# Kernel optimization log

Hardware: AMD Instinct MI355X
Metric: run time of the kernel (lower is better)

Reference implementation:

```python
import jax, jax.numpy as jnp
import numpy as np

ND = 64       # dijetFeatures (channels)
NPAIR = 6     # six dijet slots


def _interleave(x, d):
    # x: [n, nd, 12] -> [n, nd, 6, 2]; d: [n, nd, 6] -> [n, nd, 6, 1]
    n, nd, _ = x.shape
    xr = x.reshape(n, nd, NPAIR, 2)
    z = jnp.concatenate([xr, d[..., None]], axis=-1)  # [n, nd, 6, 3]
    return z


def _conv_s3(z, W, b):
    # z: [n, in, 6, 3] grouped windows; W: [out, in, 3]; stride-3 k-3 conv == per-window contraction
    return jnp.einsum('bisk,oik->bos', z, W) + b[None, :, None]  # [n, out, 6]


def setup_inputs() -> dict:
    key = jax.random.key(0)
    ks = jax.random.split(key, 8)
    n = 65536
    inp = {
        'x': jax.random.normal(ks[0], (n, ND, 12), dtype=jnp.float32),
        'd': jax.random.normal(ks[1], (n, ND, NPAIR), dtype=jnp.float32),
        'W1': jax.random.normal(ks[2], (ND, ND, 3), dtype=jnp.float32) * 0.05,
        'b1': jax.random.normal(ks[3], (ND,), dtype=jnp.float32) * 0.05,
        'W2': jax.random.normal(ks[4], (ND, ND, 3), dtype=jnp.float32) * 0.05,
        'b2': jax.random.normal(ks[5], (ND,), dtype=jnp.float32) * 0.05,
        'W3': jax.random.normal(ks[6], (ND, ND, 3), dtype=jnp.float32) * 0.05,
        'b3': jax.random.normal(ks[7], (ND,), dtype=jnp.float32) * 0.05,
    }
    return inp


def reference(x, d, W1, b1, W2, b2, W3, b3):
    d1 = d
    d = jax.nn.relu(_conv_s3(_interleave(x, d), W1, b1))
    d = jax.nn.relu(_conv_s3(_interleave(x, d), W2, b2))
    d = _conv_s3(_interleave(x, d), W3, b3)
    return jax.nn.relu(d + d1)
```

## Files before the change

### kernel.cpp

```cpp
#include <hip/hip_runtime.h>

#define ND 64
#define NPAIR 6

typedef short bf16x8 __attribute__((ext_vector_type(8)));
typedef float floatx4 __attribute__((ext_vector_type(4)));

static constexpr int SPB  = 8;
static constexpr int ROWS = SPB * NPAIR;

__device__ __forceinline__ unsigned short f2bf(float f) {
    unsigned u = __builtin_bit_cast(unsigned, f);
    u += 0x7FFFu + ((u >> 16) & 1u);
    return (unsigned short)(u >> 16);
}
__device__ __forceinline__ unsigned f2bf2(float lo, float hi) {
    return (unsigned)f2bf(lo) | ((unsigned)f2bf(hi) << 16);
}
__device__ __forceinline__ unsigned relupack2(float a, float ba, float b, float bb) {
    float u = a + ba; u = u > 0.f ? u : 0.f;
    float v = b + bb; v = v > 0.f ? v : 0.f;
    return f2bf2(u, v);
}
__device__ __forceinline__ int swzAx(int row, int c) { return (c & 8) | ((c ^ row) & 7); }
__device__ __forceinline__ int swzD (int row, int c) { return (c ^ row) & 7; }

__global__ void repack_w(const float* __restrict__ W1, const float* __restrict__ W2,
                         const float* __restrict__ W3, unsigned short* __restrict__ P) {
    int idx = blockIdx.x * 256 + threadIdx.x;
    if (idx >= 3 * 4 * 6 * 64 * 8) return;
    int j    = idx & 7;
    int lane = (idx >> 3) & 63;
    int g    = idx >> 9;
    int c    = g % 6;
    int ot   = (g / 6) & 3;
    int L    = g / 24;
    int m = lane & 15, q = lane >> 4;
    int ch = 32 * (ot >> 1) + 8 * (m >> 2) + 4 * (ot & 1) + (m & 3);
    int k  = c * 32 + q * 8 + j;
    const float* W = (L == 0) ? W1 : (L == 1) ? W2 : W3;
    float v = (k < 128) ? W[ch * 192 + (k >> 1) * 3 + (k & 1)]
                        : W[ch * 192 + (k - 128) * 3 + 2];
    P[idx] = f2bf(v);
}

__global__ __launch_bounds__(192, 5) void dijet_main(
    const float* __restrict__ x, const float* __restrict__ d,
    const float* __restrict__ b1, const float* __restrict__ b2,
    const float* __restrict__ b3, const unsigned short* __restrict__ Wa,
    float* __restrict__ out)
{
    __shared__ __align__(16) unsigned short SMEM[ROWS * 128 + ROWS * 64];
    unsigned short* Xs = SMEM;
    unsigned short* Ds = SMEM + ROWS * 128;
    float* Co = (float*)SMEM;

    const int t   = threadIdx.x;
    const int b0  = blockIdx.x * SPB;
    const int wv  = t >> 6;
    const int lane = t & 63;
    const int l15 = lane & 15;
    const int q   = lane >> 4;

    float2 dres[8];
    {
        const float2* d2 = (const float2*)(d + (size_t)b0 * 384);
        #pragma unroll
        for (int m = 0; m < 8; ++m) dres[m] = d2[m * 192 + t];
        const int i = t / 3;
        const int s = 2 * (t - 3 * (t / 3));
        #pragma unroll
        for (int m = 0; m < 8; ++m) {
            int row0 = m * 6 + s, row1 = row0 + 1;
            Ds[row0 * 64 + swzD(row0, i >> 3) * 8 + (i & 7)] = f2bf(dres[m].x);
            Ds[row1 * 64 + swzD(row1, i >> 3) * 8 + (i & 7)] = f2bf(dres[m].y);
        }
    }
    {
        const float4* x4 = (const float4*)(x + (size_t)b0 * 768);
        const int i  = t / 3;
        const int sl = (t - 3 * (t / 3)) * 2;
        const int c16 = i >> 2;
        const int iw  = i & 3;
        unsigned* Xs32 = (unsigned*)Xs;
        #pragma unroll
        for (int m = 0; m < 8; ++m) {
            float4 v = x4[m * 192 + t];
            int row0 = m * 6 + sl, row1 = row0 + 1;
            Xs32[row0 * 64 + swzAx(row0, c16) * 4 + iw] = f2bf2(v.x, v.y);
            Xs32[row1 * 64 + swzAx(row1, c16) * 4 + iw] = f2bf2(v.z, v.w);
        }
    }
    __syncthreads();

    const int r = wv * 16 + l15;
    bf16x8 Bx[4], Bd0, Bd1;
    #pragma unroll
    for (int kk = 0; kk < 4; ++kk)
        Bx[kk] = *(const bf16x8*)(Xs + r * 128 + swzAx(r, kk * 4 + q) * 8);
    Bd0 = *(const bf16x8*)(Ds + r * 64 + swzD(r, q) * 8);
    Bd1 = *(const bf16x8*)(Ds + r * 64 + swzD(r, 4 + q) * 8);

    const int rb = r / 6;
    const int rs = r - 6 * rb;

    #pragma unroll
    for (int L = 0; L < 3; ++L) {
        const float* bL = (L == 0) ? b1 : (L == 1) ? b2 : b3;
        const unsigned short* WL = Wa + L * 12288 + lane * 8;

        floatx4 acc[4];
        #pragma unroll
        for (int ot = 0; ot < 4; ++ot) {
            const unsigned short* wt = WL + ot * 3072;
            floatx4 a = {0.f, 0.f, 0.f, 0.f};
            a = __builtin_amdgcn_mfma_f32_16x16x32_bf16(*(const bf16x8*)(wt),        Bx[0], a, 0, 0, 0);
            a = __builtin_amdgcn_mfma_f32_16x16x32_bf16(*(const bf16x8*)(wt + 512),  Bx[1], a, 0, 0, 0);
            a = __builtin_amdgcn_mfma_f32_16x16x32_bf16(*(const bf16x8*)(wt + 1024), Bx[2], a, 0, 0, 0);
            a = __builtin_amdgcn_mfma_f32_16x16x32_bf16(*(const bf16x8*)(wt + 1536), Bx[3], a, 0, 0, 0);
            a = __builtin_amdgcn_mfma_f32_16x16x32_bf16(*(const bf16x8*)(wt + 2048), Bd0,   a, 0, 0, 0);
            a = __builtin_amdgcn_mfma_f32_16x16x32_bf16(*(const bf16x8*)(wt + 2560), Bd1,   a, 0, 0, 0);
            acc[ot] = a;
        }

        const float4* bv4 = (const float4*)bL;
        const float4 bl0 = bv4[2 * q],     bl1 = bv4[2 * q + 1];
        const float4 bh0 = bv4[8 + 2 * q], bh1 = bv4[8 + 2 * q + 1];

        if (L < 2) {
            union { bf16x8 h; unsigned u[4]; } p0, p1;
            p0.u[0] = relupack2(acc[0][0], bl0.x, acc[0][1], bl0.y);
            p0.u[1] = relupack2(acc[0][2], bl0.z, acc[0][3], bl0.w);
            p0.u[2] = relupack2(acc[1][0], bl1.x, acc[1][1], bl1.y);
            p0.u[3] = relupack2(acc[1][2], bl1.z, acc[1][3], bl1.w);
            p1.u[0] = relupack2(acc[2][0], bh0.x, acc[2][1], bh0.y);
            p1.u[1] = relupack2(acc[2][2], bh0.z, acc[2][3], bh0.w);
            p1.u[2] = relupack2(acc[3][0], bh1.x, acc[3][1], bh1.y);
            p1.u[3] = relupack2(acc[3][2], bh1.z, acc[3][3], bh1.w);
            Bd0 = p0.h; Bd1 = p1.h;
        } else {
            __syncthreads();
            float* cb = Co + rb * 390 + rs + (8 * q) * 6;
            cb[0]   = acc[0][0] + bl0.x; cb[6]   = acc[0][1] + bl0.y;
            cb[12]  = acc[0][2] + bl0.z; cb[18]  = acc[0][3] + bl0.w;
            cb[24]  = acc[1][0] + bl1.x; cb[30]  = acc[1][1] + bl1.y;
            cb[36]  = acc[1][2] + bl1.z; cb[42]  = acc[1][3] + bl1.w;
            cb[192] = acc[2][0] + bh0.x; cb[198] = acc[2][1] + bh0.y;
            cb[204] = acc[2][2] + bh0.z; cb[210] = acc[2][3] + bh0.w;
            cb[216] = acc[3][0] + bh1.x; cb[222] = acc[3][1] + bh1.y;
            cb[228] = acc[3][2] + bh1.z; cb[234] = acc[3][3] + bh1.w;
            __syncthreads();
            float2* out2 = (float2*)(out + (size_t)b0 * 384);
            #pragma unroll
            for (int m = 0; m < 8; ++m) {
                float2 c = *(const float2*)(Co + m * 390 + 2 * t);
                float2 rv;
                rv.x = c.x + dres[m].x; rv.x = rv.x > 0.f ? rv.x : 0.f;
                rv.y = c.y + dres[m].y; rv.y = rv.y > 0.f ? rv.y : 0.f;
                out2[m * 192 + t] = rv;
            }
        }
    }
}

extern "C" void kernel_launch(void* const* d_in, const int* in_sizes, int n_in,
                              void* d_out, int out_size, void* d_ws, size_t ws_size,
                              hipStream_t stream)
{
    const float* x  = (const float*)d_in[0];
    const float* dd = (const float*)d_in[1];
    const float* W1 = (const float*)d_in[2];
    const float* b1 = (const float*)d_in[3];
    const float* W2 = (const float*)d_in[4];
    const float* b2 = (const float*)d_in[5];
    const float* W3 = (const float*)d_in[6];
    const float* b3 = (const float*)d_in[7];
    float* out = (float*)d_out;
    unsigned short* Wp = (unsigned short*)d_ws;

    int n = in_sizes[0] / (ND * 12);

    repack_w<<<144, 256, 0, stream>>>(W1, W2, W3, Wp);
    dijet_main<<<n / SPB, 192, 0, stream>>>(x, dd, b1, b2, b3, Wp, out);
}
```

Measured before the change: 413.9 us.

## Make blocks persistent over eight sample groups with register-prefetched next-group loads

Each block now handles GRP=8 consecutive 8-sample groups in a loop instead of one. While the current group's three MFMA layers run, the next group's x and d are prefetched into registers, so global loads overlap with compute. Xs, Ds and the output staging buffer are split into separate shared arrays so the next group can be staged while outputs are written. In exchange, register pressure rises (occupancy hint drops from 5 to 3), the grid is eight times smaller, and each iteration adds an extra barrier.

```diff
diff --git a/kernel.cpp b/kernel.cpp
--- a/kernel.cpp
+++ b/kernel.cpp
@@ -8,6 +8,7 @@
 
 static constexpr int SPB  = 8;
 static constexpr int ROWS = SPB * NPAIR;
+static constexpr int GRP  = 8;
 
 __device__ __forceinline__ unsigned short f2bf(float f) {
     unsigned u = __builtin_bit_cast(unsigned, f);
@@ -44,122 +45,155 @@
     P[idx] = f2bf(v);
 }
 
-__global__ __launch_bounds__(192, 5) void dijet_main(
+__global__ __launch_bounds__(192, 3) void dijet_main(
     const float* __restrict__ x, const float* __restrict__ d,
     const float* __restrict__ b1, const float* __restrict__ b2,
     const float* __restrict__ b3, const unsigned short* __restrict__ Wa,
     float* __restrict__ out)
 {
-    __shared__ __align__(16) unsigned short SMEM[ROWS * 128 + ROWS * 64];
-    unsigned short* Xs = SMEM;
-    unsigned short* Ds = SMEM + ROWS * 128;
-    float* Co = (float*)SMEM;
-
-    const int t   = threadIdx.x;
-    const int b0  = blockIdx.x * SPB;
-    const int wv  = t >> 6;
+    __shared__ __align__(16) unsigned short Xs[ROWS * 128];
+    __shared__ __align__(16) unsigned short Ds[ROWS * 64];
+    __shared__ __align__(16) float Co[SPB * 390];
+
+    const int t    = threadIdx.x;
+    const int wv   = t >> 6;
     const int lane = t & 63;
-    const int l15 = lane & 15;
-    const int q   = lane >> 4;
-
+    const int l15  = lane & 15;
+    const int q    = lane >> 4;
+
+    const int i_d = t / 3;
+    const int s_d = 2 * (t - 3 * (t / 3));
+    const int c16 = i_d >> 2;
+    const int iw  = i_d & 3;
+    const int r   = wv * 16 + l15;
+    const int rb  = r / 6, rs = r - 6 * rb;
+
+    const size_t gbase = (size_t)blockIdx.x * (GRP * SPB);
+    const float2* d2 = (const float2*)(d + gbase * 384);
+    const float4* x4 = (const float4*)(x + gbase * 768);
+    float2* out2 = (float2*)(out + gbase * 384);
+
+    float2 dnx[8];
+    float4 xnx[8];
     float2 dres[8];
+    bf16x8 Bx[4], Bd0g, Bd1g;
+
+    #pragma unroll
+    for (int m = 0; m < 8; ++m) { dnx[m] = d2[m * 192 + t]; xnx[m] = x4[m * 192 + t]; }
     {
-        const float2* d2 = (const float2*)(d + (size_t)b0 * 384);
-        #pragma unroll
-        for (int m = 0; m < 8; ++m) dres[m] = d2[m * 192 + t];
-        const int i = t / 3;
-        const int s = 2 * (t - 3 * (t / 3));
-        #pragma unroll
-        for (int m = 0; m < 8; ++m) {
-            int row0 = m * 6 + s, row1 = row0 + 1;
-            Ds[row0 * 64 + swzD(row0, i >> 3) * 8 + (i & 7)] = f2bf(dres[m].x);
-            Ds[row1 * 64 + swzD(row1, i >> 3) * 8 + (i & 7)] = f2bf(dres[m].y);
-        }
-    }
-    {
-        const float4* x4 = (const float4*)(x + (size_t)b0 * 768);
-        const int i  = t / 3;
-        const int sl = (t - 3 * (t / 3)) * 2;
-        const int c16 = i >> 2;
-        const int iw  = i & 3;
         unsigned* Xs32 = (unsigned*)Xs;
         #pragma unroll
         for (int m = 0; m < 8; ++m) {
-            float4 v = x4[m * 192 + t];
-            int row0 = m * 6 + sl, row1 = row0 + 1;
-            Xs32[row0 * 64 + swzAx(row0, c16) * 4 + iw] = f2bf2(v.x, v.y);
-            Xs32[row1 * 64 + swzAx(row1, c16) * 4 + iw] = f2bf2(v.z, v.w);
+            int row0 = m * 6 + s_d, row1 = row0 + 1;
+            Xs32[row0 * 64 + swzAx(row0, c16) * 4 + iw] = f2bf2(xnx[m].x, xnx[m].y);
+            Xs32[row1 * 64 + swzAx(row1, c16) * 4 + iw] = f2bf2(xnx[m].z, xnx[m].w);
+            Ds[row0 * 64 + swzD(row0, i_d >> 3) * 8 + (i_d & 7)] = f2bf(dnx[m].x);
+            Ds[row1 * 64 + swzD(row1, i_d >> 3) * 8 + (i_d & 7)] = f2bf(dnx[m].y);
         }
     }
     __syncthreads();
-
-    const int r = wv * 16 + l15;
-    bf16x8 Bx[4], Bd0, Bd1;
     #pragma unroll
     for (int kk = 0; kk < 4; ++kk)
         Bx[kk] = *(const bf16x8*)(Xs + r * 128 + swzAx(r, kk * 4 + q) * 8);
-    Bd0 = *(const bf16x8*)(Ds + r * 64 + swzD(r, q) * 8);
-    Bd1 = *(const bf16x8*)(Ds + r * 64 + swzD(r, 4 + q) * 8);
-
-    const int rb = r / 6;
-    const int rs = r - 6 * rb;
-
-    #pragma unroll
-    for (int L = 0; L < 3; ++L) {
-        const float* bL = (L == 0) ? b1 : (L == 1) ? b2 : b3;
-        const unsigned short* WL = Wa + L * 12288 + lane * 8;
-
+    Bd0g = *(const bf16x8*)(Ds + r * 64 + swzD(r, q) * 8);
+    Bd1g = *(const bf16x8*)(Ds + r * 64 + swzD(r, 4 + q) * 8);
+    __syncthreads();
+    #pragma unroll
+    for (int m = 0; m < 8; ++m) dres[m] = dnx[m];
+    #pragma unroll
+    for (int m = 0; m < 8; ++m) { dnx[m] = d2[1536 + m * 192 + t]; xnx[m] = x4[1536 + m * 192 + t]; }
+
+    #pragma unroll 1
+    for (int it = 0; it < GRP; ++it) {
+        bf16x8 Bd0 = Bd0g, Bd1 = Bd1g;
         floatx4 acc[4];
+        float4 bl0f, bl1f, bh0f, bh1f;
         #pragma unroll
-        for (int ot = 0; ot < 4; ++ot) {
-            const unsigned short* wt = WL + ot * 3072;
-            floatx4 a = {0.f, 0.f, 0.f, 0.f};
-            a = __builtin_amdgcn_mfma_f32_16x16x32_bf16(*(const bf16x8*)(wt),        Bx[0], a, 0, 0, 0);
-            a = __builtin_amdgcn_mfma_f32_16x16x32_bf16(*(const bf16x8*)(wt + 512),  Bx[1], a, 0, 0, 0);
-            a = __builtin_amdgcn_mfma_f32_16x16x32_bf16(*(const bf16x8*)(wt + 1024), Bx[2], a, 0, 0, 0);
-            a = __builtin_amdgcn_mfma_f32_16x16x32_bf16(*(const bf16x8*)(wt + 1536), Bx[3], a, 0, 0, 0);
-            a = __builtin_amdgcn_mfma_f32_16x16x32_bf16(*(const bf16x8*)(wt + 2048), Bd0,   a, 0, 0, 0);
-            a = __builtin_amdgcn_mfma_f32_16x16x32_bf16(*(const bf16x8*)(wt + 2560), Bd1,   a, 0, 0, 0);
-            acc[ot] = a;
-        }
-
-        const float4* bv4 = (const float4*)bL;
-        const float4 bl0 = bv4[2 * q],     bl1 = bv4[2 * q + 1];
-        const float4 bh0 = bv4[8 + 2 * q], bh1 = bv4[8 + 2 * q + 1];
-
-        if (L < 2) {
-            union { bf16x8 h; unsigned u[4]; } p0, p1;
-            p0.u[0] = relupack2(acc[0][0], bl0.x, acc[0][1], bl0.y);
-            p0.u[1] = relupack2(acc[0][2], bl0.z, acc[0][3], bl0.w);
-            p0.u[2] = relupack2(acc[1][0], bl1.x, acc[1][1], bl1.y);
-            p0.u[3] = relupack2(acc[1][2], bl1.z, acc[1][3], bl1.w);
-            p1.u[0] = relupack2(acc[2][0], bh0.x, acc[2][1], bh0.y);
-            p1.u[1] = relupack2(acc[2][2], bh0.z, acc[2][3], bh0.w);
-            p1.u[2] = relupack2(acc[3][0], bh1.x, acc[3][1], bh1.y);
-            p1.u[3] = relupack2(acc[3][2], bh1.z, acc[3][3], bh1.w);
-            Bd0 = p0.h; Bd1 = p1.h;
-        } else {
-            __syncthreads();
+        for (int L = 0; L < 3; ++L) {
+            const float* bL = (L == 0) ? b1 : (L == 1) ? b2 : b3;
+            const unsigned short* WL = Wa + L * 12288 + lane * 8;
+            #pragma unroll
+            for (int ot = 0; ot < 4; ++ot) {
+                const unsigned short* wt = WL + ot * 3072;
+                floatx4 a = {0.f, 0.f, 0.f, 0.f};
+                a = __builtin_amdgcn_mfma_f32_16x16x32_bf16(*(const bf16x8*)(wt),        Bx[0], a, 0, 0, 0);
+                a = __builtin_amdgcn_mfma_f32_16x16x32_bf16(*(const bf16x8*)(wt + 512),  Bx[1], a, 0, 0, 0);
+                a = __builtin_amdgcn_mfma_f32_16x16x32_bf16(*(const bf16x8*)(wt + 1024), Bx[2], a, 0, 0, 0);
+                a = __builtin_amdgcn_mfma_f32_16x16x32_bf16(*(const bf16x8*)(wt + 1536), Bx[3], a, 0, 0, 0);
+                a = __builtin_amdgcn_mfma_f32_16x16x32_bf16(*(const bf16x8*)(wt + 2048), Bd0,   a, 0, 0, 0);
+                a = __builtin_amdgcn_mfma_f32_16x16x32_bf16(*(const bf16x8*)(wt + 2560), Bd1,   a, 0, 0, 0);
+                acc[ot] = a;
+            }
+            const float4* bv4 = (const float4*)bL;
+            const float4 bl0 = bv4[2 * q],     bl1 = bv4[2 * q + 1];
+            const float4 bh0 = bv4[8 + 2 * q], bh1 = bv4[8 + 2 * q + 1];
+            if (L < 2) {
+                union { bf16x8 h; unsigned u[4]; } p0, p1;
+                p0.u[0] = relupack2(acc[0][0], bl0.x, acc[0][1], bl0.y);
+                p0.u[1] = relupack2(acc[0][2], bl0.z, acc[0][3], bl0.w);
+                p0.u[2] = relupack2(acc[1][0], bl1.x, acc[1][1], bl1.y);
+                p0.u[3] = relupack2(acc[1][2], bl1.z, acc[1][3], bl1.w);
+                p1.u[0] = relupack2(acc[2][0], bh0.x, acc[2][1], bh0.y);
+                p1.u[1] = relupack2(acc[2][2], bh0.z, acc[2][3], bh0.w);
+                p1.u[2] = relupack2(acc[3][0], bh1.x, acc[3][1], bh1.y);
+                p1.u[3] = relupack2(acc[3][2], bh1.z, acc[3][3], bh1.w);
+                Bd0 = p0.h; Bd1 = p1.h;
+            } else {
+                bl0f = bl0; bl1f = bl1; bh0f = bh0; bh1f = bh1;
+            }
+        }
+
+        if (it + 1 < GRP) {
+            unsigned* Xs32 = (unsigned*)Xs;
+            #pragma unroll
+            for (int m = 0; m < 8; ++m) {
+                int row0 = m * 6 + s_d, row1 = row0 + 1;
+                Xs32[row0 * 64 + swzAx(row0, c16) * 4 + iw] = f2bf2(xnx[m].x, xnx[m].y);
+                Xs32[row1 * 64 + swzAx(row1, c16) * 4 + iw] = f2bf2(xnx[m].z, xnx[m].w);
+                Ds[row0 * 64 + swzD(row0, i_d >> 3) * 8 + (i_d & 7)] = f2bf(dnx[m].x);
+                Ds[row1 * 64 + swzD(row1, i_d >> 3) * 8 + (i_d & 7)] = f2bf(dnx[m].y);
+            }
+        }
+
+        {
             float* cb = Co + rb * 390 + rs + (8 * q) * 6;
-            cb[0]   = acc[0][0] + bl0.x; cb[6]   = acc[0][1] + bl0.y;
-            cb[12]  = acc[0][2] + bl0.z; cb[18]  = acc[0][3] + bl0.w;
-            cb[24]  = acc[1][0] + bl1.x; cb[30]  = acc[1][1] + bl1.y;
-            cb[36]  = acc[1][2] + bl1.z; cb[42]  = acc[1][3] + bl1.w;
-            cb[192] = acc[2][0] + bh0.x; cb[198] = acc[2][1] + bh0.y;
-            cb[204] = acc[2][2] + bh0.z; cb[210] = acc[2][3] + bh0.w;
-            cb[216] = acc[3][0] + bh1.x; cb[222] = acc[3][1] + bh1.y;
-            cb[228] = acc[3][2] + bh1.z; cb[234] = acc[3][3] + bh1.w;
-            __syncthreads();
-            float2* out2 = (float2*)(out + (size_t)b0 * 384);
-            #pragma unroll
-            for (int m = 0; m < 8; ++m) {
-                float2 c = *(const float2*)(Co + m * 390 + 2 * t);
-                float2 rv;
-                rv.x = c.x + dres[m].x; rv.x = rv.x > 0.f ? rv.x : 0.f;
-                rv.y = c.y + dres[m].y; rv.y = rv.y > 0.f ? rv.y : 0.f;
-                out2[m * 192 + t] = rv;
-            }
-        }
+            cb[0]   = acc[0][0] + bl0f.x; cb[6]   = acc[0][1] + bl0f.y;
+            cb[12]  = acc[0][2] + bl0f.z; cb[18]  = acc[0][3] + bl0f.w;
+            cb[24]  = acc[1][0] + bl1f.x; cb[30]  = acc[1][1] + bl1f.y;
+            cb[36]  = acc[1][2] + bl1f.z; cb[42]  = acc[1][3] + bl1f.w;
+            cb[192] = acc[2][0] + bh0f.x; cb[198] = acc[2][1] + bh0f.y;
+            cb[204] = acc[2][2] + bh0f.z; cb[210] = acc[2][3] + bh0f.w;
+            cb[216] = acc[3][0] + bh1f.x; cb[222] = acc[3][1] + bh1f.y;
+            cb[228] = acc[3][2] + bh1f.z; cb[234] = acc[3][3] + bh1f.w;
+        }
+        __syncthreads();
+
+        #pragma unroll
+        for (int m = 0; m < 8; ++m) {
+            float2 c = *(const float2*)(Co + m * 390 + 2 * t);
+            float2 rv;
+            rv.x = c.x + dres[m].x; rv.x = rv.x > 0.f ? rv.x : 0.f;
+            rv.y = c.y + dres[m].y; rv.y = rv.y > 0.f ? rv.y : 0.f;
+            out2[it * 1536 + m * 192 + t] = rv;
+        }
+
+        if (it + 1 < GRP) {
+            #pragma unroll
+            for (int kk = 0; kk < 4; ++kk)
+                Bx[kk] = *(const bf16x8*)(Xs + r * 128 + swzAx(r, kk * 4 + q) * 8);
+            Bd0g = *(const bf16x8*)(Ds + r * 64 + swzD(r, q) * 8);
+            Bd1g = *(const bf16x8*)(Ds + r * 64 + swzD(r, 4 + q) * 8);
+            #pragma unroll
+            for (int m = 0; m < 8; ++m) dres[m] = dnx[m];
+            if (it + 2 < GRP) {
+                #pragma unroll
+                for (int m = 0; m < 8; ++m) {
+                    dnx[m] = d2[(it + 2) * 1536 + m * 192 + t];
+                    xnx[m] = x4[(it + 2) * 1536 + m * 192 + t];
+                }
+            }
+        }
+        __syncthreads();
     }
 }
 
@@ -181,5 +215,5 @@
     int n = in_sizes[0] / (ND * 12);
 
     repack_w<<<144, 256, 0, stream>>>(W1, W2, W3, Wp);
-    dijet_main<<<n / SPB, 192, 0, stream>>>(x, dd, b1, b2, b3, Wp, out);
-}
+    dijet_main<<<n / (SPB * GRP), 192, 0, stream>>>(x, dd, b1, b2, b3, Wp, out);
+}
```

Result: slower. 917.6 us (+121.7%).
